# Performance work log

Measured on AMD Instinct MI355X. Metric: run time of the kernel, lower is better.

The kernel has to match this reference:

```python
import jax, jax.numpy as jnp
import numpy as np

N = 16384   # total nodes in batch
E = 65536   # edges
B = 512     # sessions
L = 32      # nodes per session
H = 64      # hidden_size
HEADS = 16  # GAT heads (layer 1)
K = 3       # interests
V = 32000   # n_node (item vocab)
NEG = 0.2   # leaky relu slope


def _u(k, shape, stdv):
    return jax.random.uniform(k, shape, jnp.float32, -stdv, stdv)


def setup_inputs():
    key = jax.random.key(0)
    ks = jax.random.split(key, 24)
    s = 1.0 / np.sqrt(H)  # reset_parameters: uniform(-stdv, stdv)
    D = K * H
    return {
        "x": jax.random.randint(ks[0], (N,), 0, V),
        "edge_index": jax.random.randint(ks[1], (2, E), 0, N),
        "batch": jnp.repeat(jnp.arange(B, dtype=jnp.int32), L),
        "embedding": _u(ks[2], (V, H), s),
        "w_interest": _u(ks[3], (H, K), s),
        "gat1_W": _u(ks[4], (K, H, HEADS * H), s),
        "gat1_as": _u(ks[5], (K, HEADS, H), s),
        "gat1_ad": _u(ks[6], (K, HEADS, H), s),
        "gat1_b": _u(ks[7], (K, HEADS * H), s),
        "gat2_W": _u(ks[8], (K, HEADS * H, H), s),
        "gat2_as": _u(ks[9], (K, 1, H), s),
        "gat2_ad": _u(ks[10], (K, 1, H), s),
        "gat2_b": _u(ks[11], (K, H), s),
        "W1_w": _u(ks[12], (D, D), s), "W1_b": _u(ks[13], (D,), s),
        "W2_w": _u(ks[14], (D, D), s), "W2_b": _u(ks[15], (D,), s),
        "q_w": _u(ks[16], (D, 1), s), "q_b": _u(ks[17], (1,), s),
        "W3_w": _u(ks[18], (2 * D, D), s), "W3_b": _u(ks[19], (D,), s),
    }


def _gat(h_in, W, b, a_s, a_d, src, dst, valid, heads, out):
    """PyG GATConv: per-head linear, edge softmax over dest, self-loops for all nodes."""
    n = h_in.shape[0]
    h = (h_in @ W).reshape(n, heads, out)          # [n, heads, out]
    asrc = (h * a_s[None]).sum(-1)                 # [n, heads]
    adst = (h * a_d[None]).sum(-1)
    loop = jnp.arange(n)
    fs = jnp.concatenate([src, loop])              # edges + self-loops
    fd = jnp.concatenate([dst, loop])
    v = jnp.concatenate([valid, jnp.ones((n,), bool)])
    logits = jax.nn.leaky_relu(asrc[fs] + adst[fd], NEG)   # [E+n, heads]
    logits = jnp.where(v[:, None], logits, -1e9)
    m = jax.ops.segment_max(logits, fd, num_segments=n)
    p = jnp.exp(logits - m[fd]) * v[:, None]
    denom = jax.ops.segment_sum(p, fd, num_segments=n)     # [n, heads]
    num = jax.ops.segment_sum(p[:, :, None] * h[fs], fd, num_segments=n)
    return (num / denom[:, :, None]).reshape(n, heads * out) + b


def _model(x, edge_index, batch, embedding, w_interest,
           gat1_W, gat1_as, gat1_ad, gat1_b,
           gat2_W, gat2_as, gat2_ad, gat2_b,
           W1_w, W1_b, W2_w, W2_b, q_w, q_b, W3_w, W3_b):
    e = embedding[x]                                # [N, H]
    g = jax.nn.softmax((e @ w_interest) / 0.1, axis=-1)   # [N, K]
    mask = g > (1.0 / K)                            # interest_mask
    src, dst = edge_index[0], edge_index[1]
    hiddens = []
    for i in range(K):                              # fixed small interest loop
        xi = g[:, i:i + 1] * e                      # einsum('ik,il->ikl')[:, i]
        valid = mask[src, i] & mask[dst, i]         # subgraph edge mask
        h1 = jax.nn.relu(_gat(xi, gat1_W[i], gat1_b[i], gat1_as[i], gat1_ad[i],
                              src, dst, valid, HEADS, H))
        h2 = _gat(h1, gat2_W[i], gat2_b[i], gat2_as[i], gat2_ad[i],
                  src, dst, valid, 1, H)
        hiddens.append(h2)
    sess = jnp.concatenate(hiddens, axis=1)         # [N, K*H]
    # Embedding2Score
    last_idx = jax.ops.segment_max(jnp.arange(N), batch, num_segments=B)
    v_n = sess[last_idx]                            # [B, K*H]  last node per session
    q1 = v_n[batch] @ W1_w + W1_b                   # v_n repeated per node
    q2 = sess @ W2_w + W2_b
    alpha = jax.nn.sigmoid(q1 + q2) @ q_w + q_b     # [N, 1]
    s_g = jax.ops.segment_sum(alpha * sess, batch, num_segments=B)
    s_h = jnp.concatenate([v_n, s_g], axis=1) @ W3_w + W3_b   # [B, K*H]
    s_h = s_h.reshape(B * K, H)                     # multi-interest split
    z = s_h @ embedding.T                           # [B*K, V]
    return z.reshape(B, K, V).max(axis=1)           # [B, V]


def reference(x, edge_index, batch, embedding, w_interest,
              gat1_W, gat1_as, gat1_ad, gat1_b,
              gat2_W, gat2_as, gat2_ad, gat2_b,
              W1_w, W1_b, W2_w, W2_b, q_w, q_b, W3_w, W3_b):
    return _model(x, edge_index, batch, embedding, w_interest,
                  gat1_W, gat1_as, gat1_ad, gat1_b,
                  gat2_W, gat2_as, gat2_ad, gat2_b,
                  W1_w, W1_b, W2_w, W2_b, q_w, q_b, W3_w, W3_b)
```

## Files before the change

kernel.cpp:

```cpp
#include <hip/hip_runtime.h>
#include <math.h>

#define NN 16384
#define EE 65536
#define BB 512
#define VV 32000

typedef unsigned short us_t;
typedef unsigned int u32_t;
typedef __attribute__((ext_vector_type(4))) float f32x4;
typedef __attribute__((ext_vector_type(8))) short bf16x8;
typedef __attribute__((ext_vector_type(4))) unsigned int u32x4;

__device__ __forceinline__ float bf2f(unsigned int u) {
  return __uint_as_float((u & 0xffffu) << 16);
}
__device__ __forceinline__ unsigned short f2bf(float f) {
  unsigned int x = __float_as_uint(f);
  unsigned int r = (x + 0x7fffu + ((x >> 16) & 1u)) >> 16;
  return (unsigned short)r;
}
__device__ __forceinline__ bf16x8 ntld(const us_t* p) {
  return __builtin_nontemporal_load((const bf16x8*)p);
}
__device__ __forceinline__ void ntst(us_t* p, u32_t a, u32_t b, u32_t c, u32_t d) {
  u32x4 v = {a, b, c, d};
  __builtin_nontemporal_store(v, (u32x4*)p);
}
__device__ __forceinline__ float wsum(float v) {
#pragma unroll
  for (int o = 32; o; o >>= 1) v += __shfl_xor(v, o, 64);
  return v;
}
__device__ __forceinline__ float redu16(float v) {
  v += __shfl_xor(v, 1, 64);
  v += __shfl_xor(v, 2, 64);
  v += __shfl_xor(v, 4, 64);
  v += __shfl_xor(v, 8, 64);
  return v;
}
__device__ __forceinline__ float lrelu(float x) { return x > 0.f ? x : 0.2f * x; }

__global__ void k_detect(const void* emb, int* flag) {
  if (threadIdx.x == 0 && blockIdx.x == 0) {
    const us_t* u = (const us_t*)emb;
    int ok = 1;
    for (int i = 0; i < 128; i++) {
      float v = bf2f((unsigned int)u[i]);
      if (!(fabsf(v) <= 0.13f)) { ok = 0; break; }
    }
    *flag = ok;
  }
}

struct PrepArgs {
  const void* src[17];
  void* dst[17];
  int n[17];
  int kind[17];
  int start[18];
};

__global__ void k_prep(PrepArgs pa, const int* __restrict__ flag) {
  int blk = blockIdx.x;
  int s = 0;
  while (s < 16 && blk >= pa.start[s + 1]) s++;
  int i = (blk - pa.start[s]) * 256 + threadIdx.x;
  if (i >= pa.n[s]) return;
  float v = (*flag) ? bf2f((unsigned int)((const us_t*)pa.src[s])[i])
                    : ((const float*)pa.src[s])[i];
  int kind = pa.kind[s];
  if (kind == 0) {
    ((float*)pa.dst[s])[i] = v;
  } else if (kind == 1) {
    ((us_t*)pa.dst[s])[i] = f2bf(v);
  } else if (kind == 2) {
    int ii = i >> 16, r = i & 65535, k = r >> 10, col = r & 1023;
    ((us_t*)pa.dst[s])[(ii << 16) + col * 64 + k] = f2bf(v);
  } else if (kind == 3) {
    int ii = i >> 16, r = i & 65535, k = r >> 6, col = r & 63;
    ((us_t*)pa.dst[s])[(ii << 16) + col * 1024 + k] = f2bf(v);
  } else {
    int k = i / 192, col = i % 192;
    ((us_t*)pa.dst[s])[col * 192 + k] = f2bf(v);
  }
}

__global__ void k_prepWa(const void* __restrict__ g1Wraw,
                         const float* __restrict__ g1as, const float* __restrict__ g1ad,
                         const int* __restrict__ flag, us_t* __restrict__ Waspack) {
  int gid = blockIdx.x * 256 + threadIdx.x;
  if (gid >= 96 * 64) return;
  int c = gid >> 6, k = gid & 63;
  int i = c >> 5, sd = (c >> 4) & 1, h = c & 15;
  const float* av = (sd ? g1ad : g1as) + i * 1024 + h * 64;
  size_t base = (size_t)i * 65536 + (size_t)k * 1024 + h * 64;
  int isbf = *flag;
  float s = 0.f;
  for (int d = 0; d < 64; d++) {
    float wv = isbf ? bf2f((unsigned int)((const us_t*)g1Wraw)[base + d])
                    : ((const float*)g1Wraw)[base + d];
    s += wv * av[d];
  }
  Waspack[c * 64 + k] = f2bf(s);
}

__global__ void k_embed(const int* __restrict__ x, const void* __restrict__ embr,
                        const void* __restrict__ wintr, const int* __restrict__ flag,
                        us_t* __restrict__ e_bf, float* __restrict__ g) {
  int gid = blockIdx.x * blockDim.x + threadIdx.x;
  int n = gid >> 6, lane = gid & 63;
  if (n >= NN) return;
  int isbf = *flag;
  size_t ei = (size_t)x[n] * 64 + lane;
  float v = isbf ? bf2f((unsigned int)((const us_t*)embr)[ei]) : ((const float*)embr)[ei];
  e_bf[(size_t)n * 64 + lane] = f2bf(v);
  float w0, w1, w2;
  if (isbf) {
    const us_t* w = (const us_t*)wintr;
    w0 = bf2f(w[lane * 3 + 0]); w1 = bf2f(w[lane * 3 + 1]); w2 = bf2f(w[lane * 3 + 2]);
  } else {
    const float* w = (const float*)wintr;
    w0 = w[lane * 3 + 0]; w1 = w[lane * 3 + 1]; w2 = w[lane * 3 + 2];
  }
  float t0 = wsum(v * w0), t1 = wsum(v * w1), t2 = wsum(v * w2);
  if (lane == 0) {
    float l0 = t0 / 0.1f, l1 = t1 / 0.1f, l2 = t2 / 0.1f;
    float m = fmaxf(l0, fmaxf(l1, l2));
    float p0 = __expf(l0 - m), p1 = __expf(l1 - m), p2 = __expf(l2 - m);
    float inv = 1.0f / (p0 + p1 + p2);
    g[n * 4 + 0] = p0 * inv; g[n * 4 + 1] = p1 * inv;
    g[n * 4 + 2] = p2 * inv; g[n * 4 + 3] = 0.f;
  }
}

__global__ void k_countv(const int* __restrict__ ei, const float* __restrict__ g,
                         int* __restrict__ countsv) {
  int e = blockIdx.x * 256 + threadIdx.x;
  if (e >= EE) return;
  int s = ei[e], d = ei[EE + e];
  const float thr = 1.0f / 3.0f;
#pragma unroll
  for (int i = 0; i < 3; i++) {
    if (g[s * 4 + i] > thr && g[d * 4 + i] > thr)
      atomicAdd(&countsv[i * NN + d], 1);
  }
}

__global__ void k_scanv(const int* __restrict__ counts, int* __restrict__ offsets) {
  __shared__ int part[256];
  __shared__ int excl[257];
  int t = threadIdx.x;
  int base = t * 192;
  int s = 0;
  for (int j = 0; j < 192; j++) s += counts[base + j];
  part[t] = s;
  __syncthreads();
  if (t == 0) {
    int run = 0;
    for (int j = 0; j < 256; j++) { excl[j] = run; run += part[j]; }
    excl[256] = run;
  }
  __syncthreads();
  int run = excl[t];
  for (int j = 0; j < 192; j++) { offsets[base + j] = run; run += counts[base + j]; }
  if (t == 255) offsets[3 * NN] = excl[256];
}

__global__ void k_fillv(const int* __restrict__ ei, const float* __restrict__ g,
                        const float* __restrict__ eatt,
                        const int* __restrict__ offsetsv, int* __restrict__ fillposv,
                        int2* __restrict__ edgesC, float* __restrict__ easrcP) {
  int e = blockIdx.x * 256 + threadIdx.x;
  if (e >= EE) return;
  int s = ei[e], d = ei[EE + e];
  const float thr = 1.0f / 3.0f;
#pragma unroll
  for (int i = 0; i < 3; i++) {
    float gs = g[s * 4 + i];
    if (gs > thr && g[d * 4 + i] > thr) {
      int pos = offsetsv[i * NN + d] + atomicAdd(&fillposv[i * NN + d], 1);
      edgesC[pos] = make_int2(s, __float_as_int(gs));
      const float* er = &eatt[(size_t)s * 96 + i * 32];
      float* op = &easrcP[(size_t)pos * 16];
#pragma unroll
      for (int h = 0; h < 16; h++) op[h] = gs * er[h];
    }
  }
}

__global__ __launch_bounds__(256) void k_easrc(
    const us_t* __restrict__ e_bf, const us_t* __restrict__ Waspack,
    float* __restrict__ eatt) {
  __shared__ char As[8192];
  int t = threadIdx.x;
  int row0 = blockIdx.x * 64;
  for (int id = t; id < 512; id += 256) {
    int r = id >> 3, c = id & 7;
    uint4 v = *(const uint4*)&e_bf[(size_t)(row0 + r) * 64 + c * 8];
    *(uint4*)(As + r * 128 + ((c ^ (r & 7)) << 4)) = v;
  }
  __syncthreads();
  int wv = t >> 6, L = t & 63, li = L & 15, lq = L >> 4;
#pragma unroll
  for (int ct = 0; ct < 6; ct++) {
    f32x4 acc = {0.f, 0.f, 0.f, 0.f};
#pragma unroll
    for (int ks = 0; ks < 2; ks++) {
      int row = wv * 16 + li;
      bf16x8 af = *(const bf16x8*)(As + row * 128 + (((ks * 4 + lq) ^ (row & 7)) << 4));
      bf16x8 bfr = *(const bf16x8*)(Waspack + (size_t)(ct * 16 + li) * 64 + ks * 32 + lq * 8);
      acc = __builtin_amdgcn_mfma_f32_16x16x32_bf16(af, bfr, acc, 0, 0, 0);
    }
#pragma unroll
    for (int r = 0; r < 4; r++) {
      int row = row0 + wv * 16 + lq * 4 + r;
      eatt[(size_t)row * 96 + ct * 16 + li] = acc[r];
    }
  }
}

__global__ __launch_bounds__(256) void k_phaseA(
    const us_t* __restrict__ e_bf, const float* __restrict__ g,
    const float* __restrict__ eatt,
    const int* __restrict__ offsetsv, const int2* __restrict__ edgesC,
    const float* __restrict__ easrcP, us_t* __restrict__ xagg) {
  int t = threadIdx.x;
  int intr = blockIdx.y;
  int wv = t >> 6, L = t & 63;
  int n = blockIdx.x * 4 + wv;
  int h = L >> 2;
  int doff = (L & 3) * 16;
  float gn = g[n * 4 + intr];
  float ad = gn * eatt[(size_t)n * 96 + intr * 32 + 16 + h];
  float m = lrelu(gn * eatt[(size_t)n * 96 + intr * 32 + h] + ad);
  float den = 1.f;
  float acc[16];
  {
    const uint4* ep = (const uint4*)&e_bf[(size_t)n * 64 + doff];
    uint4 a = ep[0], b = ep[1];
    acc[0] = gn * bf2f(a.x);  acc[1] = gn * bf2f(a.x >> 16);
    acc[2] = gn * bf2f(a.y);  acc[3] = gn * bf2f(a.y >> 16);
    acc[4] = gn * bf2f(a.z);  acc[5] = gn * bf2f(a.z >> 16);
    acc[6] = gn * bf2f(a.w);  acc[7] = gn * bf2f(a.w >> 16);
    acc[8] = gn * bf2f(b.x);  acc[9] = gn * bf2f(b.x >> 16);
    acc[10] = gn * bf2f(b.y); acc[11] = gn * bf2f(b.y >> 16);
    acc[12] = gn * bf2f(b.z); acc[13] = gn * bf2f(b.z >> 16);
    acc[14] = gn * bf2f(b.w); acc[15] = gn * bf2f(b.w >> 16);
  }
  int beg = offsetsv[intr * NN + n], end = offsetsv[intr * NN + n + 1];
  for (int j = beg; j < end; j++) {
    int2 sg = edgesC[j];
    int s = sg.x;
    float gs = __int_as_float(sg.y);
    float l = lrelu(easrcP[(size_t)j * 16 + h] + ad);
    float p = __expf(l - m);
    den += p;
    float pg = p * gs;
    const uint4* ep = (const uint4*)&e_bf[(size_t)s * 64 + doff];
    uint4 a = ep[0], b = ep[1];
    acc[0] += pg * bf2f(a.x);  acc[1] += pg * bf2f(a.x >> 16);
    acc[2] += pg * bf2f(a.y);  acc[3] += pg * bf2f(a.y >> 16);
    acc[4] += pg * bf2f(a.z);  acc[5] += pg * bf2f(a.z >> 16);
    acc[6] += pg * bf2f(a.w);  acc[7] += pg * bf2f(a.w >> 16);
    acc[8] += pg * bf2f(b.x);  acc[9] += pg * bf2f(b.x >> 16);
    acc[10] += pg * bf2f(b.y); acc[11] += pg * bf2f(b.y >> 16);
    acc[12] += pg * bf2f(b.z); acc[13] += pg * bf2f(b.z >> 16);
    acc[14] += pg * bf2f(b.w); acc[15] += pg * bf2f(b.w >> 16);
  }
  float inv = 1.f / den;
  u32_t w[8];
#pragma unroll
  for (int kk = 0; kk < 8; kk++) {
    w[kk] = (u32_t)f2bf(acc[2 * kk] * inv) | ((u32_t)f2bf(acc[2 * kk + 1] * inv) << 16);
  }
  us_t* op = &xagg[(((size_t)intr * 16 + h) * NN + n) * 64 + doff];
  ntst(op, w[0], w[1], w[2], w[3]);
  ntst(op + 8, w[4], w[5], w[6], w[7]);
}

__global__ __launch_bounds__(256) void k_h2gemm(
    const us_t* __restrict__ xagg, const us_t* __restrict__ g1Wt,
    const us_t* __restrict__ g2Wt, const float* __restrict__ b1all,
    const float* __restrict__ g2as, const float* __restrict__ g2ad,
    float* __restrict__ h2pre_a, float* __restrict__ a2s, float* __restrict__ a2d) {
  __shared__ char As[16384];
  __shared__ char Bs[16384];
  __shared__ char Ts[16384];
  __shared__ float b1s[1024];
  int t = threadIdx.x;
  int intr = blockIdx.y;
  int row0 = blockIdx.x * 64;
  const us_t* Wt1 = g1Wt + (size_t)intr * 65536;
  const us_t* Wt2 = g2Wt + (size_t)intr * 65536;
  const float* a_s = g2as + intr * 64;
  const float* a_d = g2ad + intr * 64;
  float* h2pre = h2pre_a + (size_t)intr * NN * 64;
  for (int id = t; id < 1024; id += 256) b1s[id] = b1all[intr * 1024 + id];
  int wv = t >> 6, lane = t & 63, li = lane & 15, lq = lane >> 4;
  f32x4 acc[4];
#pragma unroll
  for (int sub = 0; sub < 4; sub++) acc[sub] = {0.f, 0.f, 0.f, 0.f};
  for (int kb = 0; kb < 8; kb++) {
    int h0 = kb * 2;
    __syncthreads();
    for (int id = t; id < 1024; id += 256) {
      int r = id >> 4, c = id & 15;
      int hh = c >> 3, d = (c & 7) * 8;
      bf16x8 v = ntld(&xagg[(((size_t)intr * 16 + h0 + hh) * NN + row0 + r) * 64 + d]);
      *(bf16x8*)(As + r * 256 + ((c ^ (r & 15)) << 4)) = v;
      uint4 w = *(const uint4*)&Wt2[(size_t)r * 1024 + kb * 128 + c * 8];
      *(uint4*)(Bs + r * 256 + ((c ^ (r & 15)) << 4)) = w;
    }
    __syncthreads();
#pragma unroll
    for (int hh = 0; hh < 2; hh++) {
      int h = h0 + hh;
      f32x4 c1[4];
#pragma unroll
      for (int ct = 0; ct < 4; ct++) c1[ct] = {0.f, 0.f, 0.f, 0.f};
#pragma unroll
      for (int ks = 0; ks < 2; ks++) {
        int r = wv * 16 + li;
        int ca = hh * 8 + ks * 4 + lq;
        bf16x8 af = *(const bf16x8*)(As + r * 256 + ((ca ^ (r & 15)) << 4));
#pragma unroll
        for (int ct = 0; ct < 4; ct++) {
          bf16x8 bfr = *(const bf16x8*)&Wt1[(size_t)(h * 64 + ct * 16 + li) * 64 + ks * 32 + lq * 8];
          c1[ct] = __builtin_amdgcn_mfma_f32_16x16x32_bf16(af, bfr, c1[ct], 0, 0, 0);
        }
      }
#pragma unroll
      for (int ct = 0; ct < 4; ct++) {
        float bv = b1s[h * 64 + ct * 16 + li];
#pragma unroll
        for (int r = 0; r < 4; r++) {
          int row = wv * 16 + lq * 4 + r;
          int byte = (hh * 64 + ct * 16 + li) * 2;
          float tv = fmaxf(c1[ct][r] + bv, 0.f);
          *(us_t*)(Ts + row * 256 + (((byte >> 4) ^ (row & 15)) << 4) + (byte & 15)) = f2bf(tv);
        }
      }
    }
#pragma unroll
    for (int ks = 0; ks < 4; ks++) {
      int r = wv * 16 + li;
      bf16x8 af = *(const bf16x8*)(Ts + r * 256 + ((((ks << 2) | lq) ^ (r & 15)) << 4));
#pragma unroll
      for (int sub = 0; sub < 4; sub++) {
        int vr = sub * 16 + li;
        bf16x8 bf_ = *(const bf16x8*)(Bs + vr * 256 + ((((ks << 2) | lq) ^ (vr & 15)) << 4));
        acc[sub] = __builtin_amdgcn_mfma_f32_16x16x32_bf16(af, bf_, acc[sub], 0, 0, 0);
      }
    }
  }
  float asv[4], adv[4];
#pragma unroll
  for (int sub = 0; sub < 4; sub++) {
    asv[sub] = a_s[sub * 16 + li];
    adv[sub] = a_d[sub * 16 + li];
  }
#pragma unroll
  for (int rr = 0; rr < 4; rr++) {
    int n = row0 + wv * 16 + lq * 4 + rr;
    float s = 0.f, d = 0.f;
#pragma unroll
    for (int sub = 0; sub < 4; sub++) {
      float hv = acc[sub][rr];
      h2pre[(size_t)n * 64 + sub * 16 + li] = hv;
      s += hv * asv[sub];
      d += hv * adv[sub];
    }
    s = redu16(s); d = redu16(d);
    if (li == 0) {
      a2s[(size_t)intr * NN + n] = s;
      a2d[(size_t)intr * NN + n] = d;
    }
  }
}

__global__ void k_gat2_agg(const float* __restrict__ h2pre_a,
                           const float* __restrict__ a2s_a, const float* __restrict__ a2d_a,
                           const float* __restrict__ b2all,
                           const int* __restrict__ offsetsv,
                           const int2* __restrict__ edgesC, float* __restrict__ sess) {
  int intr = blockIdx.y;
  int gid = blockIdx.x * blockDim.x + threadIdx.x;
  int n = gid >> 6, lane = gid & 63;
  if (n >= NN) return;
  const float* h2pre = h2pre_a + (size_t)intr * NN * 64;
  const float* a2s = a2s_a + (size_t)intr * NN;
  const float* a2d = a2d_a + (size_t)intr * NN;
  const float* b2 = b2all + intr * 64;
  float ad = a2d[n];
  float m = lrelu(a2s[n] + ad);
  float den = 1.f;
  float acc = h2pre[(size_t)n * 64 + lane];
  int beg = offsetsv[intr * NN + n], end = offsetsv[intr * NN + n + 1];
  for (int j = beg; j < end; j++) {
    int s = edgesC[j].x;
    float l = lrelu(a2s[s] + ad);
    float p = __expf(l - m);
    den += p;
    acc += p * h2pre[(size_t)s * 64 + lane];
  }
  sess[(size_t)n * 192 + intr * 64 + lane] = acc / den + b2[lane];
}

__global__ __launch_bounds__(192) void k_vq1(
    const float* __restrict__ sess,
    const float* __restrict__ W1w, const float* __restrict__ W1b,
    float* __restrict__ vn, float* __restrict__ vq1) {
  __shared__ float row[192];
  int b = blockIdx.x, j = threadIdx.x;
  int li = b * 32 + 31;
  float v = sess[(size_t)li * 192 + j];
  row[j] = v;
  vn[b * 192 + j] = v;
  __syncthreads();
  float acc = W1b[j];
  for (int k = 0; k < 192; k++) acc += row[k] * W1w[k * 192 + j];
  vq1[b * 192 + j] = acc;
}

__global__ __launch_bounds__(256) void k_alpha_sg_mfma(
    const float* __restrict__ sess, const float* __restrict__ vq1,
    const us_t* __restrict__ W2T, const float* __restrict__ W2b,
    const float* __restrict__ qw, const float* __restrict__ qb,
    float* __restrict__ sg) {
  __shared__ char As[64 * 512];
  __shared__ float vq_l[2 * 192];
  __shared__ float w2b_l[192], qw_l[192];
  __shared__ float sg_l[2 * 192];
  int t = threadIdx.x;
  int n0 = blockIdx.x * 64;
  if (t < 192) { w2b_l[t] = W2b[t]; qw_l[t] = qw[t]; }
  for (int id = t; id < 384; id += 256) {
    sg_l[id] = 0.f;
    vq_l[id] = vq1[(size_t)(blockIdx.x * 2) * 192 + id];
  }
  for (int id = t; id < 1536; id += 256) {
    int r = id / 24, c = id % 24;
    const float* p = &sess[(size_t)(n0 + r) * 192 + c * 8];
    float4 f0 = *(const float4*)p;
    float4 f1 = *(const float4*)(p + 4);
    u32_t w0 = (u32_t)f2bf(f0.x) | ((u32_t)f2bf(f0.y) << 16);
    u32_t w1 = (u32_t)f2bf(f0.z) | ((u32_t)f2bf(f0.w) << 16);
    u32_t w2 = (u32_t)f2bf(f1.x) | ((u32_t)f2bf(f1.y) << 16);
    u32_t w3 = (u32_t)f2bf(f1.z) | ((u32_t)f2bf(f1.w) << 16);
    *(uint4*)(As + r * 512 + ((c ^ (r & 7)) << 4)) = make_uint4(w0, w1, w2, w3);
  }
  __syncthreads();
  int wv = t >> 6, lane = t & 63, li = lane & 15, lq = lane >> 4;
  int sl = wv >> 1;
  f32x4 acc[12];
#pragma unroll
  for (int sub = 0; sub < 12; sub++) acc[sub] = {0.f, 0.f, 0.f, 0.f};
#pragma unroll
  for (int ks = 0; ks < 6; ks++) {
    int r = wv * 16 + li;
    bf16x8 af = *(const bf16x8*)(As + r * 512 + (((ks * 4 + lq) ^ (r & 7)) << 4));
#pragma unroll
    for (int sub = 0; sub < 12; sub++) {
      bf16x8 bfr = *(const bf16x8*)&W2T[(size_t)(sub * 16 + li) * 192 + ks * 32 + lq * 8];
      acc[sub] = __builtin_amdgcn_mfma_f32_16x16x32_bf16(af, bfr, acc[sub], 0, 0, 0);
    }
  }
  float qbv = qb[0];
  float s_part[12];
#pragma unroll
  for (int sub = 0; sub < 12; sub++) s_part[sub] = 0.f;
#pragma unroll
  for (int rr = 0; rr < 4; rr++) {
    int n = n0 + wv * 16 + lq * 4 + rr;
    float ap = 0.f;
    float sv[12];
#pragma unroll
    for (int sub = 0; sub < 12; sub++) {
      int col = sub * 16 + li;
      float q = vq_l[sl * 192 + col] + acc[sub][rr] + w2b_l[col];
      float sgm = 1.f / (1.f + __expf(-q));
      ap += sgm * qw_l[col];
      sv[sub] = sess[(size_t)n * 192 + col];
    }
    ap = redu16(ap);
    float alpha = ap + qbv;
#pragma unroll
    for (int sub = 0; sub < 12; sub++) s_part[sub] += alpha * sv[sub];
  }
#pragma unroll
  for (int sub = 0; sub < 12; sub++) {
    float v = s_part[sub];
    v += __shfl_xor(v, 16, 64);
    v += __shfl_xor(v, 32, 64);
    if (lq == 0) atomicAdd(&sg_l[sl * 192 + sub * 16 + li], v);
  }
  __syncthreads();
  for (int id = t; id < 384; id += 256)
    sg[(size_t)(blockIdx.x * 2) * 192 + id] = sg_l[id];
}

__global__ __launch_bounds__(192) void k_sh(
    const float* __restrict__ vn, const float* __restrict__ sg,
    const float* __restrict__ W3w, const float* __restrict__ W3b,
    float* __restrict__ sh) {
  __shared__ float row[384];
  int b = blockIdx.x, j = threadIdx.x;
  row[j] = vn[b * 192 + j];
  row[192 + j] = sg[b * 192 + j];
  __syncthreads();
  float acc = W3b[j];
  for (int k = 0; k < 384; k++) acc += row[k] * W3w[k * 192 + j];
  sh[b * 192 + j] = acc;
}

__global__ __launch_bounds__(256) void k_final_mfma(
    const float* __restrict__ sh, const us_t* __restrict__ emb_bf,
    void* __restrict__ out, const int* __restrict__ flag) {
  __shared__ uint4 AsU[384];
  __shared__ uint4 BsU[2048];
  char* As = (char*)AsU;
  char* Bs = (char*)BsU;
  int t = threadIdx.x;
  int v0 = blockIdx.x * 256, b0 = blockIdx.y * 16;
  for (int id = t; id < 384; id += 256) {
    int i2 = id >> 7, rem = id & 127, r = rem >> 3, c = rem & 7;
    const float* p = &sh[(size_t)(b0 + r) * 192 + i2 * 64 + c * 8];
    float4 f0 = *(const float4*)p;
    float4 f1 = *(const float4*)(p + 4);
    u32_t w0 = (u32_t)f2bf(f0.x) | ((u32_t)f2bf(f0.y) << 16);
    u32_t w1 = (u32_t)f2bf(f0.z) | ((u32_t)f2bf(f0.w) << 16);
    u32_t w2 = (u32_t)f2bf(f1.x) | ((u32_t)f2bf(f1.y) << 16);
    u32_t w3 = (u32_t)f2bf(f1.z) | ((u32_t)f2bf(f1.w) << 16);
    *(uint4*)(As + i2 * 2048 + r * 128 + ((c ^ (r & 7)) << 4)) = make_uint4(w0, w1, w2, w3);
  }
  for (int id = t; id < 2048; id += 256) {
    int vr = id >> 3, c = id & 7;
    uint4 v = *(const uint4*)&emb_bf[(size_t)(v0 + vr) * 64 + c * 8];
    *(uint4*)(Bs + vr * 128 + ((c ^ (vr & 7)) << 4)) = v;
  }
  __syncthreads();
  int wv = t >> 6, lane = t & 63, li = lane & 15, lq = lane >> 4;
  int cb = wv * 64;
  int isbf = *flag;
  f32x4 acc[3][4];
#pragma unroll
  for (int i = 0; i < 3; i++)
#pragma unroll
    for (int sub = 0; sub < 4; sub++) acc[i][sub] = {0.f, 0.f, 0.f, 0.f};
#pragma unroll
  for (int ks = 0; ks < 2; ks++) {
    bf16x8 bfr[4];
#pragma unroll
    for (int sub = 0; sub < 4; sub++) {
      int vr = cb + sub * 16 + li;
      bfr[sub] = *(const bf16x8*)(Bs + vr * 128 + ((((ks << 2) | lq) ^ (vr & 7)) << 4));
    }
#pragma unroll
    for (int i = 0; i < 3; i++) {
      bf16x8 af = *(const bf16x8*)(As + i * 2048 + li * 128 + ((((ks << 2) | lq) ^ (li & 7)) << 4));
#pragma unroll
      for (int sub = 0; sub < 4; sub++)
        acc[i][sub] = __builtin_amdgcn_mfma_f32_16x16x32_bf16(af, bfr[sub], acc[i][sub], 0, 0, 0);
    }
  }
#pragma unroll
  for (int sub = 0; sub < 4; sub++) {
    int col = v0 + cb + sub * 16 + li;
#pragma unroll
    for (int rr = 0; rr < 4; rr++) {
      float o = fmaxf(fmaxf(acc[0][sub][rr], acc[1][sub][rr]), acc[2][sub][rr]);
      int b = b0 + lq * 4 + rr;
      if (isbf) ((us_t*)out)[(size_t)b * VV + col] = f2bf(o);
      else ((float*)out)[(size_t)b * VV + col] = o;
    }
  }
}

extern "C" void kernel_launch(void* const* d_in, const int* in_sizes, int n_in,
                              void* d_out, int out_size, void* d_ws, size_t ws_size,
                              hipStream_t stream) {
  if (n_in < 21) return;
  const int* x = (const int*)d_in[0];
  const int* ei = (const int*)d_in[1];

  char* ws = (char*)d_ws;
  size_t off = 0;
  auto A = [&](size_t bytes) -> char* {
    char* p = ws + off;
    off += (bytes + 255) & ~(size_t)255;
    return p;
  };
  int* flag = (int*)A(4);
  us_t* emb_bf = (us_t*)A((size_t)VV * 64 * 2);
  us_t* e_bf = (us_t*)A((size_t)NN * 64 * 2);
  us_t* g1Wt = (us_t*)A((size_t)3 * 65536 * 2);
  us_t* g2Wt = (us_t*)A((size_t)3 * 65536 * 2);
  us_t* W2T = (us_t*)A((size_t)36864 * 2);
  us_t* Waspack = (us_t*)A((size_t)96 * 64 * 2);
  float* eatt = (float*)A((size_t)NN * 96 * 4);
  float* c_g1as = (float*)A(3072 * 4);
  float* c_g1ad = (float*)A(3072 * 4);
  float* c_g1b = (float*)A(3072 * 4);
  float* c_g2as = (float*)A(192 * 4);
  float* c_g2ad = (float*)A(192 * 4);
  float* c_g2b = (float*)A(192 * 4);
  float* c_W1w = (float*)A(36864 * 4);
  float* c_W1b = (float*)A(192 * 4);
  float* c_W2b = (float*)A(192 * 4);
  float* c_qw = (float*)A(192 * 4);
  float* c_qb = (float*)A(4);
  float* c_W3w = (float*)A(73728 * 4);
  float* c_W3b = (float*)A(192 * 4);
  float* g_buf = (float*)A((size_t)NN * 4 * 4);
  us_t* xagg = (us_t*)A((size_t)3 * NN * 1024 * 2);
  float* h2pre = (float*)A((size_t)3 * NN * 64 * 4);
  float* a2s = (float*)A((size_t)3 * NN * 4);
  float* a2d = (float*)A((size_t)3 * NN * 4);
  float* sess = (float*)A((size_t)NN * 192 * 4);
  float* vq1 = (float*)A((size_t)BB * 192 * 4);
  float* sg = (float*)A((size_t)BB * 192 * 4);
  float* vn = (float*)A((size_t)BB * 192 * 4);
  float* shb = (float*)A((size_t)BB * 192 * 4);
  int* countsv = (int*)A((size_t)3 * NN * 4);
  int* offsetsv = (int*)A((size_t)(3 * NN + 1) * 4);
  int* fillposv = (int*)A((size_t)3 * NN * 4);
  int2* edgesC = (int2*)A((size_t)3 * EE * 8);
  float* easrcP = (float*)A((size_t)3 * EE * 16 * 4);
  if (off > ws_size) return;

  hipMemsetAsync(countsv, 0, 3 * NN * 4, stream);
  hipMemsetAsync(fillposv, 0, 3 * NN * 4, stream);

  k_detect<<<1, 64, 0, stream>>>(d_in[3], flag);

  PrepArgs pa;
  int nb = 0, idx = 0;
  auto SEC = [&](const void* s, void* d, int n, int kind) {
    pa.src[idx] = s; pa.dst[idx] = d; pa.n[idx] = n; pa.kind[idx] = kind;
    pa.start[idx] = nb; nb += (n + 255) / 256; idx++;
  };
  SEC(d_in[3], emb_bf, VV * 64, 1);
  SEC(d_in[5], g1Wt, 196608, 2);
  SEC(d_in[9], g2Wt, 196608, 3);
  SEC(d_in[15], W2T, 36864, 4);
  SEC(d_in[6], c_g1as, 3072, 0);
  SEC(d_in[7], c_g1ad, 3072, 0);
  SEC(d_in[8], c_g1b, 3072, 0);
  SEC(d_in[10], c_g2as, 192, 0);
  SEC(d_in[11], c_g2ad, 192, 0);
  SEC(d_in[12], c_g2b, 192, 0);
  SEC(d_in[13], c_W1w, 36864, 0);
  SEC(d_in[14], c_W1b, 192, 0);
  SEC(d_in[16], c_W2b, 192, 0);
  SEC(d_in[17], c_qw, 192, 0);
  SEC(d_in[18], c_qb, 1, 0);
  SEC(d_in[19], c_W3w, 73728, 0);
  SEC(d_in[20], c_W3b, 192, 0);
  pa.start[17] = nb;
  k_prep<<<nb, 256, 0, stream>>>(pa, flag);
  k_prepWa<<<24, 256, 0, stream>>>(d_in[5], c_g1as, c_g1ad, flag, Waspack);

  k_embed<<<NN * 64 / 256, 256, 0, stream>>>(x, d_in[3], d_in[4], flag, e_bf, g_buf);
  k_easrc<<<NN / 64, 256, 0, stream>>>(e_bf, Waspack, eatt);
  k_countv<<<EE / 256, 256, 0, stream>>>(ei, g_buf, countsv);
  k_scanv<<<1, 256, 0, stream>>>(countsv, offsetsv);
  k_fillv<<<EE / 256, 256, 0, stream>>>(ei, g_buf, eatt, offsetsv, fillposv,
                                        edgesC, easrcP);

  k_phaseA<<<dim3(NN / 4, 3), 256, 0, stream>>>(
      e_bf, g_buf, eatt, offsetsv, edgesC, easrcP, xagg);
  k_h2gemm<<<dim3(NN / 64, 3), 256, 0, stream>>>(
      xagg, g1Wt, g2Wt, c_g1b, c_g2as, c_g2ad, h2pre, a2s, a2d);
  k_gat2_agg<<<dim3(NN * 64 / 256, 3), 256, 0, stream>>>(
      h2pre, a2s, a2d, c_g2b, offsetsv, edgesC, sess);

  k_vq1<<<BB, 192, 0, stream>>>(sess, c_W1w, c_W1b, vn, vq1);
  k_alpha_sg_mfma<<<NN / 64, 256, 0, stream>>>(sess, vq1, W2T, c_W2b, c_qw, c_qb, sg);
  k_sh<<<BB, 192, 0, stream>>>(vn, sg, c_W3w, c_W3b, shb);
  k_final_mfma<<<dim3(VV / 256, BB / 16), 256, 0, stream>>>(shb, emb_bf, d_out, flag);
}
```

Measured before the change: 268.0 us.

## Double-buffer xagg tile via registers and read W2 fragments directly from global

```diff
diff --git a/kernel.cpp b/kernel.cpp
--- a/kernel.cpp
+++ b/kernel.cpp
@@ -284,8 +284,7 @@
     const us_t* __restrict__ g2Wt, const float* __restrict__ b1all,
     const float* __restrict__ g2as, const float* __restrict__ g2ad,
     float* __restrict__ h2pre_a, float* __restrict__ a2s, float* __restrict__ a2d) {
-  __shared__ char As[16384];
-  __shared__ char Bs[16384];
+  __shared__ char As[2][16384];
   __shared__ char Ts[16384];
   __shared__ float b1s[1024];
   int t = threadIdx.x;
@@ -298,21 +297,37 @@
   float* h2pre = h2pre_a + (size_t)intr * NN * 64;
   for (int id = t; id < 1024; id += 256) b1s[id] = b1all[intr * 1024 + id];
   int wv = t >> 6, lane = t & 63, li = lane & 15, lq = lane >> 4;
+  bf16x8 vreg[4];
+  int rr_[4], cc_[4];
+#pragma unroll
+  for (int j = 0; j < 4; j++) {
+    int id = t + j * 256;
+    rr_[j] = id >> 4;
+    cc_[j] = id & 15;
+  }
+  auto LOADX = [&](int kb) {
+    int h0 = kb * 2;
+#pragma unroll
+    for (int j = 0; j < 4; j++) {
+      int hh = cc_[j] >> 3, d = (cc_[j] & 7) * 8;
+      vreg[j] = ntld(&xagg[(((size_t)intr * 16 + h0 + hh) * NN + row0 + rr_[j]) * 64 + d]);
+    }
+  };
+  auto WRITEX = [&](char* dst) {
+#pragma unroll
+    for (int j = 0; j < 4; j++)
+      *(bf16x8*)(dst + rr_[j] * 256 + ((cc_[j] ^ (rr_[j] & 15)) << 4)) = vreg[j];
+  };
   f32x4 acc[4];
 #pragma unroll
   for (int sub = 0; sub < 4; sub++) acc[sub] = {0.f, 0.f, 0.f, 0.f};
+  LOADX(0);
+  WRITEX(&As[0][0]);
+  __syncthreads();
   for (int kb = 0; kb < 8; kb++) {
+    if (kb + 1 < 8) LOADX(kb + 1);
     int h0 = kb * 2;
-    __syncthreads();
-    for (int id = t; id < 1024; id += 256) {
-      int r = id >> 4, c = id & 15;
-      int hh = c >> 3, d = (c & 7) * 8;
-      bf16x8 v = ntld(&xagg[(((size_t)intr * 16 + h0 + hh) * NN + row0 + r) * 64 + d]);
-      *(bf16x8*)(As + r * 256 + ((c ^ (r & 15)) << 4)) = v;
-      uint4 w = *(const uint4*)&Wt2[(size_t)r * 1024 + kb * 128 + c * 8];
-      *(uint4*)(Bs + r * 256 + ((c ^ (r & 15)) << 4)) = w;
-    }
-    __syncthreads();
+    char* A_ = &As[kb & 1][0];
 #pragma unroll
     for (int hh = 0; hh < 2; hh++) {
       int h = h0 + hh;
@@ -323,7 +338,7 @@
       for (int ks = 0; ks < 2; ks++) {
         int r = wv * 16 + li;
         int ca = hh * 8 + ks * 4 + lq;
-        bf16x8 af = *(const bf16x8*)(As + r * 256 + ((ca ^ (r & 15)) << 4));
+        bf16x8 af = *(const bf16x8*)(A_ + r * 256 + ((ca ^ (r & 15)) << 4));
 #pragma unroll
         for (int ct = 0; ct < 4; ct++) {
           bf16x8 bfr = *(const bf16x8*)&Wt1[(size_t)(h * 64 + ct * 16 + li) * 64 + ks * 32 + lq * 8];
@@ -349,9 +364,13 @@
 #pragma unroll
       for (int sub = 0; sub < 4; sub++) {
         int vr = sub * 16 + li;
-        bf16x8 bf_ = *(const bf16x8*)(Bs + vr * 256 + ((((ks << 2) | lq) ^ (vr & 15)) << 4));
+        bf16x8 bf_ = *(const bf16x8*)&Wt2[(size_t)vr * 1024 + kb * 128 + ((ks << 2) | lq) * 8];
         acc[sub] = __builtin_amdgcn_mfma_f32_16x16x32_bf16(af, bf_, acc[sub], 0, 0, 0);
       }
+    }
+    if (kb + 1 < 8) {
+      WRITEX(&As[(kb + 1) & 1][0]);
+      __syncthreads();
     }
   }
   float asv[4], adv[4];
```

Result: slower. 302.0 us (+12.7%).

## Split h2gemm K-loop across two blocks with atomic accumulation

Applied to the files above, without the earlier changes.

```diff
diff --git a/kernel.cpp b/kernel.cpp
--- a/kernel.cpp
+++ b/kernel.cpp
@@ -282,26 +282,24 @@
 __global__ __launch_bounds__(256) void k_h2gemm(
     const us_t* __restrict__ xagg, const us_t* __restrict__ g1Wt,
     const us_t* __restrict__ g2Wt, const float* __restrict__ b1all,
-    const float* __restrict__ g2as, const float* __restrict__ g2ad,
-    float* __restrict__ h2pre_a, float* __restrict__ a2s, float* __restrict__ a2d) {
+    float* __restrict__ h2pre_a) {
   __shared__ char As[16384];
   __shared__ char Bs[16384];
   __shared__ char Ts[16384];
   __shared__ float b1s[1024];
   int t = threadIdx.x;
   int intr = blockIdx.y;
+  int z = blockIdx.z;
   int row0 = blockIdx.x * 64;
   const us_t* Wt1 = g1Wt + (size_t)intr * 65536;
   const us_t* Wt2 = g2Wt + (size_t)intr * 65536;
-  const float* a_s = g2as + intr * 64;
-  const float* a_d = g2ad + intr * 64;
   float* h2pre = h2pre_a + (size_t)intr * NN * 64;
   for (int id = t; id < 1024; id += 256) b1s[id] = b1all[intr * 1024 + id];
   int wv = t >> 6, lane = t & 63, li = lane & 15, lq = lane >> 4;
   f32x4 acc[4];
 #pragma unroll
   for (int sub = 0; sub < 4; sub++) acc[sub] = {0.f, 0.f, 0.f, 0.f};
-  for (int kb = 0; kb < 8; kb++) {
+  for (int kb = z * 4; kb < z * 4 + 4; kb++) {
     int h0 = kb * 2;
     __syncthreads();
     for (int id = t; id < 1024; id += 256) {
@@ -354,28 +352,28 @@
       }
     }
   }
-  float asv[4], adv[4];
-#pragma unroll
-  for (int sub = 0; sub < 4; sub++) {
-    asv[sub] = a_s[sub * 16 + li];
-    adv[sub] = a_d[sub * 16 + li];
-  }
 #pragma unroll
   for (int rr = 0; rr < 4; rr++) {
     int n = row0 + wv * 16 + lq * 4 + rr;
-    float s = 0.f, d = 0.f;
-#pragma unroll
-    for (int sub = 0; sub < 4; sub++) {
-      float hv = acc[sub][rr];
-      h2pre[(size_t)n * 64 + sub * 16 + li] = hv;
-      s += hv * asv[sub];
-      d += hv * adv[sub];
-    }
-    s = redu16(s); d = redu16(d);
-    if (li == 0) {
-      a2s[(size_t)intr * NN + n] = s;
-      a2d[(size_t)intr * NN + n] = d;
-    }
+#pragma unroll
+    for (int sub = 0; sub < 4; sub++)
+      atomicAdd(&h2pre[(size_t)n * 64 + sub * 16 + li], acc[sub][rr]);
+  }
+}
+
+__global__ void k_a2dots(const float* __restrict__ h2pre_a,
+                         const float* __restrict__ g2as, const float* __restrict__ g2ad,
+                         float* __restrict__ a2s, float* __restrict__ a2d) {
+  int intr = blockIdx.y;
+  int gid = blockIdx.x * blockDim.x + threadIdx.x;
+  int n = gid >> 6, lane = gid & 63;
+  if (n >= NN) return;
+  float hv = h2pre_a[((size_t)intr * NN + n) * 64 + lane];
+  float s = wsum(hv * g2as[intr * 64 + lane]);
+  float d = wsum(hv * g2ad[intr * 64 + lane]);
+  if (lane == 0) {
+    a2s[(size_t)intr * NN + n] = s;
+    a2d[(size_t)intr * NN + n] = d;
   }
 }
 
@@ -631,6 +629,7 @@
 
   hipMemsetAsync(countsv, 0, 3 * NN * 4, stream);
   hipMemsetAsync(fillposv, 0, 3 * NN * 4, stream);
+  hipMemsetAsync(h2pre, 0, (size_t)3 * NN * 64 * 4, stream);
 
   k_detect<<<1, 64, 0, stream>>>(d_in[3], flag);
 
@@ -670,8 +669,10 @@
 
   k_phaseA<<<dim3(NN / 4, 3), 256, 0, stream>>>(
       e_bf, g_buf, eatt, offsetsv, edgesC, easrcP, xagg);
-  k_h2gemm<<<dim3(NN / 64, 3), 256, 0, stream>>>(
-      xagg, g1Wt, g2Wt, c_g1b, c_g2as, c_g2ad, h2pre, a2s, a2d);
+  k_h2gemm<<<dim3(NN / 64, 3, 2), 256, 0, stream>>>(
+      xagg, g1Wt, g2Wt, c_g1b, h2pre);
+  k_a2dots<<<dim3(NN * 64 / 256, 3), 256, 0, stream>>>(
+      h2pre, c_g2as, c_g2ad, a2s, a2d);
   k_gat2_agg<<<dim3(NN * 64 / 256, 3), 256, 0, stream>>>(
       h2pre, a2s, a2d, c_g2b, offsetsv, edgesC, sess);
 
```

Measured after the change: 285.4 us. 1.07x slower.
